# Kernel tuning notes

Measured on AMD Instinct MI355X. Metric: run time of the kernel, lower is better.

Reference implementation:

```python
import jax, jax.numpy as jnp
import numpy as np

THRESHOLD = 0.35      # overlap_thresh
NEGPOS_RATIO = 7
VAR0, VAR1 = 0.1, 0.2  # self.variance


def make_priors():
    # Standard RetinaFace 640x640 anchor grid -> 16800 priors (cx, cy, w, h)
    img = 640
    steps = [8, 16, 32]
    min_sizes = [[16, 32], [64, 128], [256, 512]]
    out = []
    for step, ms in zip(steps, min_sizes):
        f = img // step
        ii, jj = np.meshgrid(np.arange(f), np.arange(f), indexing="ij")
        cx = ((jj + 0.5) * step / img).ravel().astype(np.float32)
        cy = ((ii + 0.5) * step / img).ravel().astype(np.float32)
        for m in ms:
            s = np.full_like(cx, m / img)
            out.append(np.stack([cx, cy, s, s], axis=-1))
    return jnp.asarray(np.concatenate(out, axis=0), dtype=jnp.float32)


def jaccard(a, b):
    # a: [O,4] point-form gt boxes, b: [P,4] point-form priors -> IoU [O,P]
    lt = jnp.maximum(a[:, None, :2], b[None, :, :2])
    rb = jnp.minimum(a[:, None, 2:], b[None, :, 2:])
    wh = jnp.clip(rb - lt, 0.0)
    inter = wh[..., 0] * wh[..., 1]
    area_a = ((a[:, 2] - a[:, 0]) * (a[:, 3] - a[:, 1]))[:, None]
    area_b = ((b[:, 2] - b[:, 0]) * (b[:, 3] - b[:, 1]))[None, :]
    return inter / (area_a + area_b - inter)


def setup_inputs() -> dict:
    key = jax.random.key(0)
    ks = jax.random.split(key, 7)
    B, P, O = 64, 16800, 64
    loc_data = jax.random.normal(ks[0], (B, P, 4), jnp.float32)
    conf_data = jax.random.normal(ks[1], (B, P, 2), jnp.float32)
    landm_data = jax.random.normal(ks[2], (B, P, 10), jnp.float32)
    priors = make_priors()
    # targets: [B, O, 15] = [xmin ymin xmax ymax | 10 landmark coords | label]
    c = jax.random.uniform(ks[3], (B, O, 2), minval=0.15, maxval=0.85)
    wh = jax.random.uniform(ks[4], (B, O, 2), minval=0.05, maxval=0.3)
    boxes = jnp.concatenate([jnp.clip(c - wh / 2, 1e-3, 0.999),
                             jnp.clip(c + wh / 2, 1e-3, 0.999)], axis=-1)
    landms = jax.random.uniform(ks[5], (B, O, 10))
    lab = jnp.where(jax.random.uniform(ks[6], (B, O, 1)) < 0.8, 1.0, -1.0)
    targets = jnp.concatenate([boxes, landms, lab], axis=-1).astype(jnp.float32)
    return {"loc_data": loc_data, "conf_data": conf_data,
            "landm_data": landm_data, "priors": priors, "targets": targets}


def _smooth_l1(x):
    ax = jnp.abs(x)
    return jnp.where(ax < 1.0, 0.5 * ax * ax, ax - 0.5)


def reference(loc_data, conf_data, landm_data, priors, targets):
    B, P, C = conf_data.shape
    O = targets.shape[1]
    priors_pf = jnp.concatenate([priors[:, :2] - priors[:, 2:] * 0.5,
                                 priors[:, :2] + priors[:, 2:] * 0.5], axis=1)

    def match_one(t):
        truths = t[:, :4]
        landms = t[:, 4:14]
        labels = t[:, 14].astype(jnp.int32)
        ov = jaccard(truths, priors_pf)               # [O,P]
        bp_ov = ov.max(axis=1)                         # best prior per truth
        bp_idx = jnp.argmax(ov, axis=1)
        valid = bp_ov >= 0.2                           # RetinaFace gt filter
        bt_ov = ov.max(axis=0)                         # best truth per prior
        bt_idx = jnp.argmax(ov, axis=0)
        # index_fill_(best_prior_idx, 2) for valid gts, ensure best prior kept
        bt_ov = bt_ov.at[bp_idx].set(jnp.where(valid, 2.0, bt_ov[bp_idx]))
        bt_idx = bt_idx.at[bp_idx].set(jnp.arange(O))
        matched = truths[bt_idx]                       # [P,4] point form
        conf = labels[bt_idx]
        conf = jnp.where(bt_ov < THRESHOLD, 0, conf)
        # encode loc target
        g_cxcy = ((matched[:, :2] + matched[:, 2:]) * 0.5 - priors[:, :2]) / (VAR0 * priors[:, 2:])
        g_wh = jnp.log((matched[:, 2:] - matched[:, :2]) / priors[:, 2:]) / VAR1
        loc = jnp.concatenate([g_cxcy, g_wh], axis=1)
        # encode landmark target (5 points)
        ml = landms[bt_idx].reshape(P, 5, 2)
        lm = ((ml - priors[:, None, :2]) / (VAR0 * priors[:, None, 2:])).reshape(P, 10)
        any_valid = jnp.any(valid)                     # early-return branch of match()
        return (jnp.where(any_valid, loc, 0.0),
                jnp.where(any_valid, conf, 0),
                jnp.where(any_valid, lm, 0.0))

    loc_t, conf_t, landm_t = jax.vmap(match_one)(targets)
    loc_t = jax.lax.stop_gradient(loc_t)       # targets built from .data in torch
    landm_t = jax.lax.stop_gradient(landm_t)

    # landmark loss over conf_t > 0
    pos1 = conf_t > 0
    N1 = jnp.maximum(pos1.sum().astype(jnp.float32), 1.0)
    loss_landm = jnp.sum(jnp.where(pos1[..., None], _smooth_l1(landm_data - landm_t), 0.0))

    # localization loss over conf_t != 0 (labels -1 and 1 both positive)
    pos = conf_t != 0
    conf_t1 = jnp.where(pos, 1, conf_t)        # conf_t[pos] = 1 -> values in {0,1}
    loss_l = jnp.sum(jnp.where(pos[..., None], _smooth_l1(loc_data - loc_t), 0.0))

    # hard negative mining
    lse = jax.nn.logsumexp(conf_data, axis=2)                       # [B,P]
    picked = jnp.take_along_axis(conf_data, conf_t1[..., None], axis=2)[..., 0]
    ce_all = lse - picked                                            # per-anchor CE
    rank_score = jnp.where(pos, 0.0, ce_all)
    loss_idx = jnp.argsort(-rank_score, axis=1)
    idx_rank = jnp.argsort(loss_idx, axis=1)
    num_pos = pos.sum(axis=1, keepdims=True)
    num_neg = jnp.minimum(NEGPOS_RATIO * num_pos, P - 1)
    neg = idx_rank < num_neg
    union = pos | neg
    loss_c = jnp.sum(jnp.where(union, ce_all, 0.0))

    N = jnp.maximum(num_pos.sum().astype(jnp.float32), 1.0)
    return loss_l / N, loss_c / N, loss_landm / N1
```

## Files before the change

### kernel.cpp

```cpp
#include <hip/hip_runtime.h>
#include <math.h>

#define B 64
#define P 16800
#define O 64
#define THRESH 0.35f
#define VALID_T 0.2f
#define HB 2048
#define HSHIFT 21
#define CCAP 4096
#define MULT 2
#define CHB (MULT * 256)
#define NB2 ((P + CHB - 1) / CHB)
#define KD1B (B * NB2)
#define KB2B (B * O / 4)

__device__ __forceinline__ float smooth_l1(float x) {
    float ax = fabsf(x);
    return ax < 1.f ? 0.5f * ax * ax : ax - 0.5f;
}
__device__ __forceinline__ float lse2(float c0, float c1) {
    float m = fmaxf(c0, c1);
    return m + __logf(__expf(c0 - m) + __expf(c1 - m));
}
__device__ __forceinline__ void iou_upd(float4 t, float area_a,
                                        float px1, float py1, float px2, float py2,
                                        float area_b,
                                        float& bnum, float& bden, int& bio, int o) {
    float w = fmaxf(fminf(t.z, px2) - fmaxf(t.x, px1), 0.f);
    float h = fmaxf(fminf(t.w, py2) - fmaxf(t.y, py1), 0.f);
    float inter = w * h;
    float den = area_a + area_b - inter;
    if (inter * bden > bnum * den) { bnum = inter; bden = den; bio = o; }
}
__device__ __forceinline__ float wave_sum(float v) {
#pragma unroll
    for (int s = 32; s > 0; s >>= 1) v += __shfl_down(v, s, 64);
    return v;
}
__device__ __forceinline__ int wave_sum_i(int v) {
#pragma unroll
    for (int s = 32; s > 0; s >>= 1) v += __shfl_down(v, s, 64);
    return v;
}
__device__ __forceinline__ float wave_min(float v) {
#pragma unroll
    for (int s = 32; s > 0; s >>= 1) v = fminf(v, __shfl_xor(v, s, 64));
    return v;
}
__device__ __forceinline__ float wave_max(float v) {
#pragma unroll
    for (int s = 32; s > 0; s >>= 1) v = fmaxf(v, __shfl_xor(v, s, 64));
    return v;
}

__global__ void __launch_bounds__(256) kMain(
        const float* __restrict__ loc_data, const float* __restrict__ conf_data,
        const float* __restrict__ landm_data, const float* __restrict__ priors,
        const float* __restrict__ targets,
        float* __restrict__ rank, int* __restrict__ hist,
        int* __restrict__ num_pos, float* __restrict__ pos_ce,
        float* __restrict__ gsum, int* __restrict__ np1_tot,
        unsigned long long* __restrict__ bp_final) {
    if (blockIdx.x >= KD1B) {
        int pair = (blockIdx.x - KD1B) * 4 + (threadIdx.x >> 6);
        int lane = threadIdx.x & 63;
        int o = pair & (O - 1);
        int b = pair >> 6;
        const float* tt = &targets[(b * O + o) * 15];
        float tx1 = tt[0], ty1 = tt[1], tx2 = tt[2], ty2 = tt[3];
        float area_a = (tx2 - tx1) * (ty2 - ty1);
        float4 tb = make_float4(tx1, ty1, tx2, ty2);
        float bn = 0.f, bd = 1.f;
        unsigned bp = 0u;
        const int fs[6]   = {80, 80, 40, 40, 20, 20};
        const int ms[6]   = {16, 32, 64, 128, 256, 512};
        const int base[6] = {0, 6400, 12800, 14400, 16000, 16400};
#pragma unroll
        for (int c = 0; c < 6; ++c) {
            int f = fs[c];
            float inv = (float)f;
            float h = (float)ms[c] * (0.5f / 640.f);
            int j0 = (int)floorf((tx1 - h) * inv - 0.5f) - 1; if (j0 < 0) j0 = 0;
            int j1 = (int)ceilf((tx2 + h) * inv - 0.5f) + 1;  if (j1 > f - 1) j1 = f - 1;
            int i0 = (int)floorf((ty1 - h) * inv - 0.5f) - 1; if (i0 < 0) i0 = 0;
            int i1 = (int)ceilf((ty2 + h) * inv - 0.5f) + 1;  if (i1 > f - 1) i1 = f - 1;
            if (j1 < j0 || i1 < i0) continue;
            int nj = j1 - j0 + 1;
            int n = (i1 - i0 + 1) * nj;
            float rcp_nj = 1.0f / (float)nj;
            for (int idx = lane; idx < n; idx += 64) {
                int ii = (int)((float)idx * rcp_nj);
                int jj = idx - ii * nj;
                if (jj < 0) { ii--; jj += nj; } else if (jj >= nj) { ii++; jj -= nj; }
                int p = base[c] + (i0 + ii) * f + (j0 + jj);
                float4 q = ((const float4*)priors)[p];
                float px1 = q.x - q.z * 0.5f, py1 = q.y - q.w * 0.5f;
                float px2 = q.x + q.z * 0.5f, py2 = q.y + q.w * 0.5f;
                float areab = (px2 - px1) * (py2 - py1);
                float w = fmaxf(fminf(tb.z, px2) - fmaxf(tb.x, px1), 0.f);
                float hh = fmaxf(fminf(tb.w, py2) - fmaxf(tb.y, py1), 0.f);
                float inter = w * hh;
                float den = area_a + areab - inter;
                float l = bn * den, r = inter * bd;
                if (r > l) { bn = inter; bd = den; bp = (unsigned)p; }
            }
        }
#pragma unroll
        for (int s = 32; s > 0; s >>= 1) {
            float no = __shfl_xor(bn, s, 64), dd = __shfl_xor(bd, s, 64);
            unsigned po = __shfl_xor(bp, s, 64);
            float l = bn * dd, r = no * bd;
            bool take = (r > l) || (r == l && po < bp);
            if (take) { bn = no; bd = dd; bp = po; }
        }
        if (lane == 0) {
            float iou = bn / bd;
            bp_final[b * O + o] = ((unsigned long long)__float_as_uint(iou) << 32)
                                | (unsigned)(0xFFFFFFFFu - bp);
        }
        return;
    }
    int blk = blockIdx.x % NB2;
    int b = blockIdx.x / NB2;
    int p0 = blk * CHB;
    __shared__ float4 t4[O];
    __shared__ float ta[O], lab[O];
    __shared__ float lm[O][10];
    __shared__ int lhist[HB];
    __shared__ float4 wbb[4];
    __shared__ int alist[O];
    __shared__ int s_cnt;
    __shared__ float wredf[3][4];
    __shared__ int wredi[2][4];
    int tid = threadIdx.x;
    if (tid < O) {
        const float* t = &targets[(b * O + tid) * 15];
        float a0 = t[0], a1 = t[1], a2 = t[2], a3 = t[3];
        t4[tid] = make_float4(a0, a1, a2, a3);
        ta[tid] = (a2 - a0) * (a3 - a1);
        lab[tid] = t[14];
    }
    for (int i = tid; i < O * 10; i += 256)
        lm[i / 10][i % 10] = targets[b * O * 15 + (i / 10) * 15 + 4 + (i % 10)];
    for (int i = tid; i < HB; i += 256) lhist[i] = 0;
    float px1[MULT], py1[MULT], px2[MULT], py2[MULT], areab[MULT];
    float4 pr4[MULT];
    float bnum[MULT], bden[MULT]; int bi[MULT]; bool act[MULT];
    float bx1 = 1e30f, by1 = 1e30f, bx2 = -1e30f, by2 = -1e30f;
#pragma unroll
    for (int mi = 0; mi < MULT; ++mi) {
        int p = p0 + mi * 256 + tid;
        act[mi] = (p < P);
        int pc = act[mi] ? p : (P - 1);
        float4 q = ((const float4*)priors)[pc];
        pr4[mi] = q;
        px1[mi] = q.x - q.z * 0.5f; py1[mi] = q.y - q.w * 0.5f;
        px2[mi] = q.x + q.z * 0.5f; py2[mi] = q.y + q.w * 0.5f;
        areab[mi] = (px2[mi] - px1[mi]) * (py2[mi] - py1[mi]);
        bx1 = fminf(bx1, px1[mi]); by1 = fminf(by1, py1[mi]);
        bx2 = fmaxf(bx2, px2[mi]); by2 = fmaxf(by2, py2[mi]);
        bnum[mi] = 0.f; bden[mi] = 1.f; bi[mi] = 0;
    }
    bx1 = wave_min(bx1); by1 = wave_min(by1);
    bx2 = wave_max(bx2); by2 = wave_max(by2);
    int wid = tid >> 6, lid = tid & 63;
    if (lid == 0) wbb[wid] = make_float4(bx1, by1, bx2, by2);
    __syncthreads();
    if (tid < 64) {
        float ux1 = fminf(fminf(wbb[0].x, wbb[1].x), fminf(wbb[2].x, wbb[3].x));
        float uy1 = fminf(fminf(wbb[0].y, wbb[1].y), fminf(wbb[2].y, wbb[3].y));
        float ux2 = fmaxf(fmaxf(wbb[0].z, wbb[1].z), fmaxf(wbb[2].z, wbb[3].z));
        float uy2 = fmaxf(fmaxf(wbb[0].w, wbb[1].w), fmaxf(wbb[2].w, wbb[3].w));
        float4 t = t4[tid];
        bool pass = (fminf(t.z, ux2) - fmaxf(t.x, ux1) > 0.f) &&
                    (fminf(t.w, uy2) - fmaxf(t.y, uy1) > 0.f);
        unsigned long long mask = __ballot(pass);
        if (tid == 0) s_cnt = __popcll(mask);
        if (pass) {
            int pos = __popcll(mask & ((1ull << tid) - 1ull));
            alist[pos] = tid;
        }
    }
    __syncthreads();
    int cnt = s_cnt;
    for (int li = 0; li < cnt; ++li) {
        int o = alist[li];
        float4 t = t4[o];
        float w0 = fminf(t.z, bx2) - fmaxf(t.x, bx1);
        float h0 = fminf(t.w, by2) - fmaxf(t.y, by1);
        if (w0 <= 0.f || h0 <= 0.f) continue;
        float area_a = ta[o];
#pragma unroll
        for (int mi = 0; mi < MULT; ++mi)
            iou_upd(t, area_a, px1[mi], py1[mi], px2[mi], py2[mi], areab[mi],
                    bnum[mi], bden[mi], bi[mi], o);
    }
    float ll = 0.f, llm = 0.f, cep = 0.f;
    int cp = 0, cp1 = 0;
#pragma unroll
    for (int mi = 0; mi < MULT; ++mi) {
        if (!act[mi]) continue;
        int p = p0 + mi * 256 + tid;
        float best = bnum[mi] / bden[mi];
        int conf = (best >= THRESH) ? (int)lab[bi[mi]] : 0;
        float2 c01 = ((const float2*)conf_data)[b * P + p];
        float c0 = c01.x, c1 = c01.y;
        float lse = lse2(c0, c1);
        bool pos = conf != 0;
        float ce = lse - (pos ? c1 : c0);
        float rv = pos ? 0.f : ce;
        rank[(size_t)b * P + p] = rv;
        atomicAdd(&lhist[__float_as_uint(rv) >> HSHIFT], 1);
        if (pos) {
            cp++; cep += ce;
            int ti = bi[mi];
            float cx = pr4[mi].x, cy = pr4[mi].y, sw = pr4[mi].z, sh = pr4[mi].w;
            float4 t = t4[ti];
            float gx = ((t.x + t.z) * 0.5f - cx) / (0.1f * sw);
            float gy = ((t.y + t.w) * 0.5f - cy) / (0.1f * sh);
            float gw = logf((t.z - t.x) / sw) / 0.2f;
            float gh = logf((t.w - t.y) / sh) / 0.2f;
            const float* ld = &loc_data[(size_t)(b * P + p) * 4];
            ll += smooth_l1(ld[0] - gx) + smooth_l1(ld[1] - gy) +
                  smooth_l1(ld[2] - gw) + smooth_l1(ld[3] - gh);
            if (conf > 0) {
                cp1++;
                const float* lmd = &landm_data[(size_t)(b * P + p) * 10];
                for (int k5 = 0; k5 < 5; ++k5) {
                    float lx = (lm[ti][k5 * 2 + 0] - cx) / (0.1f * sw);
                    float ly = (lm[ti][k5 * 2 + 1] - cy) / (0.1f * sh);
                    llm += smooth_l1(lmd[k5 * 2 + 0] - lx) + smooth_l1(lmd[k5 * 2 + 1] - ly);
                }
            }
        }
    }
    float s_ll = wave_sum(ll), s_llm = wave_sum(llm), s_cep = wave_sum(cep);
    int s_cp = wave_sum_i(cp), s_cp1 = wave_sum_i(cp1);
    if (lid == 0) {
        wredf[0][wid] = s_ll; wredf[1][wid] = s_llm; wredf[2][wid] = s_cep;
        wredi[0][wid] = s_cp; wredi[1][wid] = s_cp1;
    }
    __syncthreads();
    if (tid == 0) {
        float ll_t = wredf[0][0] + wredf[0][1] + wredf[0][2] + wredf[0][3];
        float llm_t = wredf[1][0] + wredf[1][1] + wredf[1][2] + wredf[1][3];
        float cep_t = wredf[2][0] + wredf[2][1] + wredf[2][2] + wredf[2][3];
        int cp_t = wredi[0][0] + wredi[0][1] + wredi[0][2] + wredi[0][3];
        int cp1_t = wredi[1][0] + wredi[1][1] + wredi[1][2] + wredi[1][3];
        if (ll_t != 0.f)  atomicAdd(&gsum[0], ll_t);
        if (llm_t != 0.f) atomicAdd(&gsum[1], llm_t);
        if (cep_t != 0.f) atomicAdd(&pos_ce[b], cep_t);
        if (cp_t)  atomicAdd(&num_pos[b], cp_t);
        if (cp1_t) atomicAdd(np1_tot, cp1_t);
    }
    int* gh = hist + (size_t)b * HB;
#pragma unroll
    for (int i = tid; i < HB; i += 256) {
        int c = lhist[i];
        if (c) atomicAdd(&gh[i], c);
    }
}

__global__ void __launch_bounds__(1024) kTail(
        const float* __restrict__ priors, const float* __restrict__ targets,
        const float* __restrict__ loc_data, const float* __restrict__ conf_data,
        const float* __restrict__ landm_data,
        const unsigned long long* __restrict__ bp_final,
        float* __restrict__ rank, const int* __restrict__ hist,
        const int* __restrict__ num_pos, const float* __restrict__ pos_ce,
        float* __restrict__ gsum, int* __restrict__ np1_tot, int* __restrict__ np_tot,
        float* __restrict__ lossc_tot, int* __restrict__ done,
        float* __restrict__ out) {
    int b = blockIdx.x;
    int tid = threadIdx.x;
    __shared__ float4 t4[O];
    __shared__ float ta[O], lab[O];
    __shared__ int sp[O];
    __shared__ int lh[HB];
    __shared__ int chunkSum[256];
    __shared__ int s_np, s_bin0, s_kk0, s_cnt;
    __shared__ unsigned lcand[CCAP];
    __shared__ float wredf[16];
    __shared__ int wredi[16];
    __shared__ float s_sumgt;
    __shared__ int hist2[256];
    __shared__ int s_bin, s_kk;

    for (int i = tid; i < HB; i += 1024) lh[i] = hist[(size_t)b * HB + i];
    int p = 0, v = 0;
    if (tid < O) {
        const float* tt = &targets[(b * O + tid) * 15];
        float4 tj = make_float4(tt[0], tt[1], tt[2], tt[3]);
        t4[tid] = tj;
        ta[tid] = (tj.z - tj.x) * (tj.w - tj.y);
        lab[tid] = tt[14];
        unsigned long long kpk = bp_final[b * O + tid];
        p = (int)(0xFFFFFFFFu - (unsigned)(kpk & 0xFFFFFFFFu));
        float iou = __uint_as_float((unsigned)(kpk >> 32));
        v = (iou >= VALID_T) ? 1 : 0;
        sp[tid] = p;
    }
    if (tid == 0) s_cnt = 0;
    __syncthreads();
    int dnp = 0, dn1 = 0;
    float dll = 0.f, dllm = 0.f, dce = 0.f;
    if (tid < O) {
        int j = tid;
        bool winner = true;
        for (int jj = j + 1; jj < O; ++jj)
            if (sp[jj] == p) { winner = false; break; }
        if (winner) {
            float4 q = ((const float4*)priors)[p];
            float px1 = q.x - q.z * 0.5f, py1 = q.y - q.w * 0.5f;
            float px2 = q.x + q.z * 0.5f, py2 = q.y + q.w * 0.5f;
            float areab = (px2 - px1) * (py2 - py1);
            float bnum = 0.f, bden = 1.f; int bi = 0;
            for (int o = 0; o < O; ++o)
                iou_upd(t4[o], ta[o], px1, py1, px2, py2, areab, bnum, bden, bi, o);
            float best = bnum / bden;
            float ov_new = v ? 2.0f : best;
            int conf_old = (best >= THRESH) ? (int)lab[bi] : 0;
            int conf_new = (ov_new >= THRESH) ? (int)lab[j] : 0;
            float2 c01 = ((const float2*)conf_data)[b * P + p];
            float c0 = c01.x, c1 = c01.y;
            float lse = lse2(c0, c1);
            bool po = conf_old != 0, pn = conf_new != 0;
            float ceo = lse - (po ? c1 : c0), cen = lse - (pn ? c1 : c0);
            float rvo = po ? 0.f : ceo, rvn = pn ? 0.f : cen;
            if (__float_as_uint(rvo) != __float_as_uint(rvn)) {
                rank[(size_t)b * P + p] = rvn;
                int bo = __float_as_uint(rvo) >> HSHIFT, bn = __float_as_uint(rvn) >> HSHIFT;
                if (bo != bn) { atomicAdd(&lh[bn], 1); atomicAdd(&lh[bo], -1); }
            }
            const float* ld = &loc_data[(size_t)(b * P + p) * 4];
            auto enc_ll = [&](int ti) -> float {
                float4 t = t4[ti];
                float gx = ((t.x + t.z) * 0.5f - q.x) / (0.1f * q.z);
                float gy = ((t.y + t.w) * 0.5f - q.y) / (0.1f * q.w);
                float gw = logf((t.z - t.x) / q.z) / 0.2f;
                float gh = logf((t.w - t.y) / q.w) / 0.2f;
                return smooth_l1(ld[0] - gx) + smooth_l1(ld[1] - gy) +
                       smooth_l1(ld[2] - gw) + smooth_l1(ld[3] - gh);
            };
            if (po) dll -= enc_ll(bi);
            if (pn) dll += enc_ll(j);
            dce = (pn ? cen : 0.f) - (po ? ceo : 0.f);
            dnp = (int)pn - (int)po;
            const float* lmd = &landm_data[(size_t)(b * P + p) * 10];
            auto enc_lm = [&](int ti) -> float {
                const float* lmt = &targets[(b * O + ti) * 15 + 4];
                float sum = 0.f;
                for (int k5 = 0; k5 < 5; ++k5) {
                    float lx = (lmt[k5 * 2 + 0] - q.x) / (0.1f * q.z);
                    float ly = (lmt[k5 * 2 + 1] - q.y) / (0.1f * q.w);
                    sum += smooth_l1(lmd[k5 * 2 + 0] - lx) + smooth_l1(lmd[k5 * 2 + 1] - ly);
                }
                return sum;
            };
            if (conf_old > 0) dllm -= enc_lm(bi);
            if (conf_new > 0) dllm += enc_lm(j);
            dn1 = (int)(conf_new > 0) - (int)(conf_old > 0);
        }
    }
    float pce_reg = 0.f;
    if (tid < 64) {
        float r_ll = wave_sum(dll), r_lm = wave_sum(dllm), r_ce = wave_sum(dce);
        int r_np = wave_sum_i(dnp), r_n1 = wave_sum_i(dn1);
        if (tid == 0) {
            if (r_ll != 0.f) atomicAdd(&gsum[0], r_ll);
            if (r_lm != 0.f) atomicAdd(&gsum[1], r_lm);
            pce_reg = pos_ce[b] + r_ce;
            int np = num_pos[b] + r_np;
            s_np = np;
            atomicAdd(np_tot, np);
            if (r_n1) atomicAdd(np1_tot, r_n1);
        }
    }
    __threadfence_block();
    __syncthreads();
    int k = s_np * 7;
    if (k > P - 1) k = P - 1;
    if (tid < 256) {
        int cs = 0;
#pragma unroll
        for (int i = 0; i < HB / 256; ++i) cs += lh[tid * (HB / 256) + i];
        chunkSum[tid] = cs;
    }
    __syncthreads();
    if (tid == 0) {
        if (k <= 0) { s_bin0 = -1; s_kk0 = 0; }
        else {
            int cum = 0, bin = 0, kk = k;
            for (int c = 255; c >= 0; --c) {
                if (cum + chunkSum[c] >= k) {
                    for (int i = HB / 256 - 1; i >= 0; --i) {
                        int hv = lh[c * (HB / 256) + i];
                        if (cum + hv >= k) { bin = c * (HB / 256) + i; kk = k - cum; goto found; }
                        cum += hv;
                    }
                }
                cum += chunkSum[c];
            }
        found:
            s_bin0 = bin; s_kk0 = kk;
        }
    }
    __syncthreads();
    int bin = s_bin0;
    float topk_b = 0.f;
    if (bin >= 0) {
        unsigned lo_bound = ((unsigned)(bin + 1)) << HSHIFT;
        const float* r = rank + (size_t)b * P;
        float sumgt = 0.f;
        for (int pp = tid; pp < P; pp += 1024) {
            float val = r[pp];
            unsigned u = __float_as_uint(val);
            if (u >= lo_bound) sumgt += val;
            else if ((u >> HSHIFT) == (unsigned)bin) {
                int idx = atomicAdd(&s_cnt, 1);
                if (idx < CCAP) lcand[idx] = u;
            }
        }
        float sg = wave_sum(sumgt);
        if ((tid & 63) == 0) wredf[tid >> 6] = sg;
        __syncthreads();
        if (tid == 0) {
            float t = 0.f;
            for (int i = 0; i < 16; ++i) t += wredf[i];
            s_sumgt = t;
        }
        int m = s_cnt;
        int kk0 = s_kk0;
        bool useG = (m > CCAP);
        unsigned pref = ((unsigned)bin) << HSHIFT;
        unsigned resolved = 0xFFFFFFFFu << HSHIFT;
        int kk = kk0;
        const int shifts[3] = {13, 5, 0};
        const int nbins[3] = {256, 256, 32};
        for (int pass = 0; pass < 3; ++pass) {
            int sh = shifts[pass], nb = nbins[pass];
            for (int i = tid; i < nb; i += 1024) hist2[i] = 0;
            __syncthreads();
            if (!useG) {
                for (int i = tid; i < m; i += 1024) {
                    unsigned u = lcand[i];
                    if ((u & resolved) == pref) atomicAdd(&hist2[(u >> sh) & (nb - 1)], 1);
                }
            } else {
                for (int pp = tid; pp < P; pp += 1024) {
                    unsigned u = __float_as_uint(r[pp]);
                    if ((u & resolved) == pref) atomicAdd(&hist2[(u >> sh) & (nb - 1)], 1);
                }
            }
            __syncthreads();
            if (tid == 0) {
                int cum = 0, d = 0, kn = kk;
                for (int i = nb - 1; i >= 0; --i) {
                    if (cum + hist2[i] >= kk) { d = i; kn = kk - cum; break; }
                    cum += hist2[i];
                }
                s_bin = d; s_kk = kn;
            }
            __syncthreads();
            pref |= ((unsigned)s_bin) << sh;
            resolved |= (unsigned)(nb - 1) << sh;
            kk = s_kk;
            __syncthreads();
        }
        float tv = __uint_as_float(pref);
        float sumS = 0.f; int cntS = 0;
        if (!useG) {
            for (int i = tid; i < m; i += 1024) {
                float val = __uint_as_float(lcand[i]);
                if (val > tv) { sumS += val; cntS++; }
            }
        } else {
            for (int pp = tid; pp < P; pp += 1024) {
                unsigned u = __float_as_uint(r[pp]);
                if ((u >> HSHIFT) == (unsigned)bin) {
                    float val = __uint_as_float(u);
                    if (val > tv) { sumS += val; cntS++; }
                }
            }
        }
        float s2 = wave_sum(sumS); int c2 = wave_sum_i(cntS);
        if ((tid & 63) == 0) { wredf[tid >> 6] = s2; wredi[tid >> 6] = c2; }
        __syncthreads();
        if (tid == 0) {
            float st = 0.f; int ct = 0;
            for (int i = 0; i < 16; ++i) { st += wredf[i]; ct += wredi[i]; }
            topk_b = s_sumgt + st + (float)(kk0 - ct) * tv;
        }
    }
    if (tid == 0) {
        atomicAdd(lossc_tot, pce_reg + topk_b);
        __threadfence();
        int old = atomicAdd(done, 1);
        if (old == B - 1) {
            float g0 = atomicAdd(&gsum[0], 0.f);
            float g1 = atomicAdd(&gsum[1], 0.f);
            float lc = atomicAdd(lossc_tot, 0.f);
            int np = atomicAdd(np_tot, 0);
            int n1 = atomicAdd(np1_tot, 0);
            float N = fmaxf((float)np, 1.f);
            float N1 = fmaxf((float)n1, 1.f);
            out[0] = g0 / N;
            out[1] = lc / N;
            out[2] = g1 / N1;
        }
    }
}

extern "C" void kernel_launch(void* const* d_in, const int* in_sizes, int n_in,
                              void* d_out, int out_size, void* d_ws, size_t ws_size,
                              hipStream_t stream) {
    const float* loc_data   = (const float*)d_in[0];
    const float* conf_data  = (const float*)d_in[1];
    const float* landm_data = (const float*)d_in[2];
    const float* priors     = (const float*)d_in[3];
    const float* targets    = (const float*)d_in[4];
    float* out = (float*)d_out;

    char* ws = (char*)d_ws;
    size_t off = 0;
    auto alloc = [&](size_t bytes) -> void* {
        void* pp = ws + off;
        off += (bytes + 255) & ~(size_t)255;
        return pp;
    };
    float* rank     = (float*)alloc((size_t)B * P * 4);
    unsigned long long* bp_final = (unsigned long long*)alloc((size_t)B * O * 8);
    size_t hist_bytes = (size_t)B * HB * 4;
    char* zbase = (char*)alloc(hist_bytes);
    int* hist = (int*)zbase;
    size_t acc_bytes = (size_t)(2 * B * 4 + 64);
    char* acc = (char*)alloc(acc_bytes);
    int*   num_pos      = (int*)acc;
    float* pos_ce       = (float*)(acc + B * 4);
    float* gsum         = (float*)(acc + 2 * B * 4);
    int*   np1_tot      = (int*)(acc + 2 * B * 4 + 8);
    int*   np_tot       = (int*)(acc + 2 * B * 4 + 12);
    float* lossc_tot    = (float*)(acc + 2 * B * 4 + 16);
    int*   done         = (int*)(acc + 2 * B * 4 + 20);
    size_t zlen = (size_t)((acc + acc_bytes) - zbase);

    hipMemsetAsync(zbase, 0, zlen, stream);
    kMain<<<dim3(KD1B + KB2B), dim3(256), 0, stream>>>(loc_data, conf_data, landm_data,
                                                       priors, targets, rank, hist,
                                                       num_pos, pos_ce, gsum, np1_tot,
                                                       bp_final);
    kTail<<<dim3(B), dim3(1024), 0, stream>>>(priors, targets, loc_data, conf_data,
                                              landm_data, bp_final, rank, hist,
                                              num_pos, pos_ce, gsum, np1_tot, np_tot,
                                              lossc_tot, done, out);
}
```

Baseline: 204.7 us.

## Cache rank row in LDS and parallelize top-k bin search with wave scans

```diff
diff --git a/kernel.cpp b/kernel.cpp
--- a/kernel.cpp
+++ b/kernel.cpp
@@ -8,7 +8,6 @@
 #define VALID_T 0.2f
 #define HB 2048
 #define HSHIFT 21
-#define CCAP 4096
 #define MULT 2
 #define CHB (MULT * 256)
 #define NB2 ((P + CHB - 1) / CHB)
@@ -51,6 +50,14 @@
 __device__ __forceinline__ float wave_max(float v) {
 #pragma unroll
     for (int s = 32; s > 0; s >>= 1) v = fmaxf(v, __shfl_xor(v, s, 64));
+    return v;
+}
+__device__ __forceinline__ int wave_sufscan(int v, int lane) {
+#pragma unroll
+    for (int s = 1; s < 64; s <<= 1) {
+        int o = __shfl_down(v, s, 64);
+        if (lane + s < 64) v += o;
+    }
     return v;
 }
 
@@ -267,26 +274,34 @@
         const float* __restrict__ loc_data, const float* __restrict__ conf_data,
         const float* __restrict__ landm_data,
         const unsigned long long* __restrict__ bp_final,
-        float* __restrict__ rank, const int* __restrict__ hist,
+        const float* __restrict__ rank, const int* __restrict__ hist,
         const int* __restrict__ num_pos, const float* __restrict__ pos_ce,
         float* __restrict__ gsum, int* __restrict__ np1_tot, int* __restrict__ np_tot,
         float* __restrict__ lossc_tot, int* __restrict__ done,
         float* __restrict__ out) {
-    int b = blockIdx.x;
-    int tid = threadIdx.x;
+    __shared__ __align__(16) unsigned lrow[P];
     __shared__ float4 t4[O];
     __shared__ float ta[O], lab[O];
     __shared__ int sp[O];
     __shared__ int lh[HB];
     __shared__ int chunkSum[256];
-    __shared__ int s_np, s_bin0, s_kk0, s_cnt;
-    __shared__ unsigned lcand[CCAP];
+    __shared__ int suf[257];
+    __shared__ int waveTot[4];
+    __shared__ int hist2[256];
+    __shared__ int s_np, s_bin0, s_kk0, s_bin, s_kk;
     __shared__ float wredf[16];
     __shared__ int wredi[16];
     __shared__ float s_sumgt;
-    __shared__ int hist2[256];
-    __shared__ int s_bin, s_kk;
-
+
+    int b = blockIdx.x;
+    int tid = threadIdx.x;
+    const float* r = rank + (size_t)b * P;
+    const float4* r4 = (const float4*)r;
+    for (int i = tid; i < P / 4; i += 1024) {
+        float4 q = r4[i];
+        ((uint4*)lrow)[i] = make_uint4(__float_as_uint(q.x), __float_as_uint(q.y),
+                                       __float_as_uint(q.z), __float_as_uint(q.w));
+    }
     for (int i = tid; i < HB; i += 1024) lh[i] = hist[(size_t)b * HB + i];
     int p = 0, v = 0;
     if (tid < O) {
@@ -301,7 +316,6 @@
         v = (iou >= VALID_T) ? 1 : 0;
         sp[tid] = p;
     }
-    if (tid == 0) s_cnt = 0;
     __syncthreads();
     int dnp = 0, dn1 = 0;
     float dll = 0.f, dllm = 0.f, dce = 0.f;
@@ -329,7 +343,7 @@
             float ceo = lse - (po ? c1 : c0), cen = lse - (pn ? c1 : c0);
             float rvo = po ? 0.f : ceo, rvn = pn ? 0.f : cen;
             if (__float_as_uint(rvo) != __float_as_uint(rvn)) {
-                rank[(size_t)b * P + p] = rvn;
+                lrow[p] = __float_as_uint(rvn);
                 int bo = __float_as_uint(rvo) >> HSHIFT, bn = __float_as_uint(rvn) >> HSHIFT;
                 if (bo != bn) { atomicAdd(&lh[bn], 1); atomicAdd(&lh[bo], -1); }
             }
@@ -377,7 +391,6 @@
             if (r_n1) atomicAdd(np1_tot, r_n1);
         }
     }
-    __threadfence_block();
     __syncthreads();
     int k = s_np * 7;
     if (k > P - 1) k = P - 1;
@@ -387,40 +400,42 @@
         for (int i = 0; i < HB / 256; ++i) cs += lh[tid * (HB / 256) + i];
         chunkSum[tid] = cs;
     }
-    __syncthreads();
-    if (tid == 0) {
-        if (k <= 0) { s_bin0 = -1; s_kk0 = 0; }
-        else {
-            int cum = 0, bin = 0, kk = k;
-            for (int c = 255; c >= 0; --c) {
-                if (cum + chunkSum[c] >= k) {
-                    for (int i = HB / 256 - 1; i >= 0; --i) {
-                        int hv = lh[c * (HB / 256) + i];
-                        if (cum + hv >= k) { bin = c * (HB / 256) + i; kk = k - cum; goto found; }
-                        cum += hv;
-                    }
+    if (tid == 0) { s_bin0 = (k <= 0) ? -1 : 0; s_kk0 = (k <= 0) ? 0 : k; }
+    __syncthreads();
+    {
+        int lane = tid & 63;
+        int vv = (tid < 256) ? chunkSum[tid] : 0;
+        vv = wave_sufscan(vv, lane);
+        if (tid < 256 && lane == 0) waveTot[tid >> 6] = vv;
+        __syncthreads();
+        if (tid < 256) {
+            int after = 0;
+            for (int g = (tid >> 6) + 1; g < 4; ++g) after += waveTot[g];
+            suf[tid] = vv + after;
+            if (tid == 0) suf[256] = 0;
+        }
+        __syncthreads();
+        if (k > 0 && tid < 256) {
+            if (suf[tid] >= k && suf[tid + 1] < k) {
+                int cum = suf[tid + 1];
+                for (int i = HB / 256 - 1; i >= 0; --i) {
+                    int hv = lh[tid * (HB / 256) + i];
+                    if (cum + hv >= k) { s_bin0 = tid * (HB / 256) + i; s_kk0 = k - cum; break; }
+                    cum += hv;
                 }
-                cum += chunkSum[c];
-            }
-        found:
-            s_bin0 = bin; s_kk0 = kk;
+            }
         }
     }
     __syncthreads();
     int bin = s_bin0;
+    int kk0 = s_kk0;
     float topk_b = 0.f;
     if (bin >= 0) {
         unsigned lo_bound = ((unsigned)(bin + 1)) << HSHIFT;
-        const float* r = rank + (size_t)b * P;
         float sumgt = 0.f;
         for (int pp = tid; pp < P; pp += 1024) {
-            float val = r[pp];
-            unsigned u = __float_as_uint(val);
-            if (u >= lo_bound) sumgt += val;
-            else if ((u >> HSHIFT) == (unsigned)bin) {
-                int idx = atomicAdd(&s_cnt, 1);
-                if (idx < CCAP) lcand[idx] = u;
-            }
+            unsigned u = lrow[pp];
+            if (u >= lo_bound) sumgt += __uint_as_float(u);
         }
         float sg = wave_sum(sumgt);
         if ((tid & 63) == 0) wredf[tid >> 6] = sg;
@@ -430,9 +445,6 @@
             for (int i = 0; i < 16; ++i) t += wredf[i];
             s_sumgt = t;
         }
-        int m = s_cnt;
-        int kk0 = s_kk0;
-        bool useG = (m > CCAP);
         unsigned pref = ((unsigned)bin) << HSHIFT;
         unsigned resolved = 0xFFFFFFFFu << HSHIFT;
         int kk = kk0;
@@ -440,27 +452,31 @@
         const int nbins[3] = {256, 256, 32};
         for (int pass = 0; pass < 3; ++pass) {
             int sh = shifts[pass], nb = nbins[pass];
-            for (int i = tid; i < nb; i += 1024) hist2[i] = 0;
+            if (tid < nb) hist2[tid] = 0;
             __syncthreads();
-            if (!useG) {
-                for (int i = tid; i < m; i += 1024) {
-                    unsigned u = lcand[i];
-                    if ((u & resolved) == pref) atomicAdd(&hist2[(u >> sh) & (nb - 1)], 1);
-                }
-            } else {
-                for (int pp = tid; pp < P; pp += 1024) {
-                    unsigned u = __float_as_uint(r[pp]);
-                    if ((u & resolved) == pref) atomicAdd(&hist2[(u >> sh) & (nb - 1)], 1);
-                }
+            for (int i = tid; i < P / 4; i += 1024) {
+                uint4 u4 = ((const uint4*)lrow)[i];
+                if ((u4.x & resolved) == pref) atomicAdd(&hist2[(u4.x >> sh) & (nb - 1)], 1);
+                if ((u4.y & resolved) == pref) atomicAdd(&hist2[(u4.y >> sh) & (nb - 1)], 1);
+                if ((u4.z & resolved) == pref) atomicAdd(&hist2[(u4.z >> sh) & (nb - 1)], 1);
+                if ((u4.w & resolved) == pref) atomicAdd(&hist2[(u4.w >> sh) & (nb - 1)], 1);
             }
             __syncthreads();
-            if (tid == 0) {
-                int cum = 0, d = 0, kn = kk;
-                for (int i = nb - 1; i >= 0; --i) {
-                    if (cum + hist2[i] >= kk) { d = i; kn = kk - cum; break; }
-                    cum += hist2[i];
-                }
-                s_bin = d; s_kk = kn;
+            int lane = tid & 63;
+            int vv = (tid < nb) ? hist2[tid] : 0;
+            vv = wave_sufscan(vv, lane);
+            if (tid < nb && lane == 0) waveTot[tid >> 6] = vv;
+            __syncthreads();
+            int ng = (nb + 63) >> 6;
+            if (tid < nb) {
+                int after = 0;
+                for (int g = (tid >> 6) + 1; g < ng; ++g) after += waveTot[g];
+                suf[tid] = vv + after;
+                if (tid == 0) suf[nb] = 0;
+            }
+            __syncthreads();
+            if (tid < nb) {
+                if (suf[tid] >= kk && suf[tid + 1] < kk) { s_bin = tid; s_kk = kk - suf[tid + 1]; }
             }
             __syncthreads();
             pref |= ((unsigned)s_bin) << sh;
@@ -470,18 +486,11 @@
         }
         float tv = __uint_as_float(pref);
         float sumS = 0.f; int cntS = 0;
-        if (!useG) {
-            for (int i = tid; i < m; i += 1024) {
-                float val = __uint_as_float(lcand[i]);
+        for (int pp = tid; pp < P; pp += 1024) {
+            unsigned u = lrow[pp];
+            if ((u >> HSHIFT) == (unsigned)bin) {
+                float val = __uint_as_float(u);
                 if (val > tv) { sumS += val; cntS++; }
-            }
-        } else {
-            for (int pp = tid; pp < P; pp += 1024) {
-                unsigned u = __float_as_uint(r[pp]);
-                if ((u >> HSHIFT) == (unsigned)bin) {
-                    float val = __uint_as_float(u);
-                    if (val > tv) { sumS += val; cntS++; }
-                }
             }
         }
         float s2 = wave_sum(sumS); int c2 = wave_sum_i(cntS);
```

Result: faster. 165.2 us (-19.3%).
